# Optimization experiments

Hardware: AMD Instinct MI355X
Metric: run time of the kernel (lower is better)

Reference implementation:

```python
import jax, jax.numpy as jnp
import numpy as np

S, H = 8192, 2048


def setup_inputs() -> dict:
    key = jax.random.key(0)
    k1, k2, k3, k4, k5 = jax.random.split(key, 5)
    encoder_outputs = jax.random.normal(k1, (S, 1, H), dtype=jnp.float32)
    hidden = jax.random.normal(k2, (H,), dtype=jnp.float32)
    # nn.Linear(2H, H): weight [H, 2H], bias [H]
    lim = 1.0 / np.sqrt(2 * H)
    W_att = jax.random.uniform(k3, (H, 2 * H), dtype=jnp.float32, minval=-lim, maxval=lim)
    b_att = jax.random.uniform(k4, (H,), dtype=jnp.float32, minval=-lim, maxval=lim)
    w = jax.random.normal(k5, (1, H), dtype=jnp.float32)
    return {"encoder_outputs": encoder_outputs, "hidden": hidden,
            "W_att": W_att, "b_att": b_att, "w": w}


def reference(encoder_outputs, hidden, W_att, b_att, w):
    # Original loops over source_len: score_i = w . (Linear(cat(hidden, enc_i)))
    # Vectorized: build [S, 2H] once, one GEMM, one dot, one softmax.
    enc = encoder_outputs[:, 0, :]                      # [S, H]
    h = jnp.broadcast_to(hidden[None, :], enc.shape)    # [S, H]
    x = jnp.concatenate([h, enc], axis=1)               # [S, 2H]
    res = x @ W_att.T + b_att                           # [S, H]
    scores = res @ w[0]                                 # [S]
    attn = jax.nn.softmax(scores, axis=0)               # softmax over source_len
    return attn[None, None, :]                          # [1, 1, S]
```

## Files before the change

### kernel.cpp

```cpp
#include <hip/hip_runtime.h>
#include <math.h>

#define SS 8192
#define HH 2048
#define NBLK 256
#define NTHR 512
#define CSB 64
#define CSROWS (HH / CSB)

__device__ unsigned g_ctr = 0;
__device__ __align__(16) float g_v2[HH] = {};

__device__ __forceinline__ void grid_barrier() {
    __syncthreads();
    if (threadIdx.x == 0) {
        unsigned old = __hip_atomic_fetch_add(&g_ctr, 1u, __ATOMIC_RELAXED,
                                              __HIP_MEMORY_SCOPE_AGENT);
        unsigned target = (old / NBLK + 1u) * NBLK;
        while (__hip_atomic_load(&g_ctr, __ATOMIC_RELAXED,
                                 __HIP_MEMORY_SCOPE_AGENT) < target)
            __builtin_amdgcn_s_sleep(16);
    }
    asm volatile("" ::: "memory");
    __syncthreads();
}

__global__ __launch_bounds__(NTHR, 2) void fused_kernel(
    const float* __restrict__ enc,
    const float* __restrict__ W,
    const float* __restrict__ w,
    float* __restrict__ out,
    float* __restrict__ sc)
{
    const int b = blockIdx.x;
    const int t = threadIdx.x;

    if (b < CSB) {
        const int row0 = b * CSROWS;
        const float4* base =
            (const float4*)(W + (size_t)row0 * (2 * HH) + HH) + t;
        float4 acc = {0.f, 0.f, 0.f, 0.f};
#pragma unroll 8
        for (int j = 0; j < CSROWS; ++j) {
            float4 a = base[(size_t)j * ((2 * HH) / 4)];
            float wj = w[row0 + j];
            acc.x += wj * a.x; acc.y += wj * a.y;
            acc.z += wj * a.z; acc.w += wj * a.w;
        }
        float* dst = g_v2 + t * 4;
        atomicAdd(dst + 0, acc.x);
        atomicAdd(dst + 1, acc.y);
        atomicAdd(dst + 2, acc.z);
        atomicAdd(dst + 3, acc.w);
    }

    grid_barrier();

    __shared__ float v2s[HH];
#pragma unroll
    for (int k = 0; k < 4; ++k)
        v2s[t + k * 512] = __hip_atomic_load(&g_v2[t + k * 512],
                                             __ATOMIC_RELAXED,
                                             __HIP_MEMORY_SCOPE_AGENT);
    __syncthreads();
    {
        const int wave = t >> 6;
        const int lane = t & 63;
        const float4* v4 = (const float4*)v2s;
        float4 vf[8];
#pragma unroll
        for (int i = 0; i < 8; ++i) vf[i] = v4[lane + i * 64];

        const int row_base = b * 32 + wave * 4;
#pragma unroll
        for (int rr = 0; rr < 4; ++rr) {
            const int row = row_base + rr;
            const float4* e = (const float4*)(enc + (size_t)row * HH);
            float acc = 0.0f;
#pragma unroll
            for (int i = 0; i < 8; ++i) {
                float4 a = e[lane + i * 64];
                acc += a.x * vf[i].x + a.y * vf[i].y
                     + a.z * vf[i].z + a.w * vf[i].w;
            }
#pragma unroll
            for (int off = 32; off > 0; off >>= 1)
                acc += __shfl_down(acc, off);
            if (lane == 0)
                __hip_atomic_store(&sc[row], acc, __ATOMIC_RELAXED,
                                   __HIP_MEMORY_SCOPE_AGENT);
        }
    }

    grid_barrier();

    {
        __shared__ float red[8];
        const int lane = t & 63;
        const int wid  = t >> 6;

        float vals[16];
        float m = -INFINITY;
#pragma unroll
        for (int i = 0; i < 16; ++i) {
            vals[i] = __hip_atomic_load(&sc[t + i * 512], __ATOMIC_RELAXED,
                                        __HIP_MEMORY_SCOPE_AGENT);
            m = fmaxf(m, vals[i]);
        }
#pragma unroll
        for (int off = 1; off < 64; off <<= 1)
            m = fmaxf(m, __shfl_xor(m, off));
        if (lane == 0) red[wid] = m;
        __syncthreads();
#pragma unroll
        for (int k = 0; k < 8; ++k) m = fmaxf(m, red[k]);

        float s = 0.0f;
#pragma unroll
        for (int i = 0; i < 16; ++i)
            s += __expf(vals[i] - m);
#pragma unroll
        for (int off = 1; off < 64; off <<= 1)
            s += __shfl_xor(s, off);
        __syncthreads();
        if (lane == 0) red[wid] = s;
        __syncthreads();
        float ss = 0.0f;
#pragma unroll
        for (int k = 0; k < 8; ++k) ss += red[k];
        const float inv = 1.0f / ss;

        if (t < 32) {
            const int e = b * 32 + t;
            float sv = __hip_atomic_load(&sc[e], __ATOMIC_RELAXED,
                                         __HIP_MEMORY_SCOPE_AGENT);
            out[e] = __expf(sv - m) * inv;
        }

        if (b == NBLK - 1) {
#pragma unroll
            for (int k = 0; k < 4; ++k)
                __hip_atomic_store(&g_v2[t + k * 512], 0.0f,
                                   __ATOMIC_RELAXED,
                                   __HIP_MEMORY_SCOPE_AGENT);
        }
    }
}

extern "C" void kernel_launch(void* const* d_in, const int* in_sizes, int n_in,
                              void* d_out, int out_size, void* d_ws, size_t ws_size,
                              hipStream_t stream) {
    const float* enc   = (const float*)d_in[0];
    const float* W_att = (const float*)d_in[2];
    const float* w     = (const float*)d_in[4];

    float* out = (float*)d_out;
    float* sc  = (float*)d_ws;

    hipLaunchKernelGGL(fused_kernel, dim3(NBLK), dim3(NTHR), 0, stream,
                       enc, W_att, w, out, sc);
}
```

Baseline: 132.1 us.

## Spread W-vector reduction over all blocks and use per-block softmax partials

The W^T·w contraction is now split across all 256 blocks, each writing partial vectors to a global buffer instead of 64 blocks issuing float atomicAdds. A second grid-barrier phase then reduces those partials column-wise. The softmax now has each block compute a local max and sum, publish them as one 64-bit pair, and combine them with an online-softmax rescale, so blocks no longer re-read all 8192 scores. The grid barrier switches to a release-flag scheme that only the last arriving block writes. The cost is one extra grid barrier and a 2 MB partial buffer.

```diff
diff --git a/kernel.cpp b/kernel.cpp
--- a/kernel.cpp
+++ b/kernel.cpp
@@ -5,21 +5,27 @@
 #define HH 2048
 #define NBLK 256
 #define NTHR 512
-#define CSB 64
-#define CSROWS (HH / CSB)
 
 __device__ unsigned g_ctr = 0;
-__device__ __align__(16) float g_v2[HH] = {};
+__device__ unsigned g_rel = 0;
+__device__ float g_part[NBLK][HH];
+__device__ float g_v2[HH];
+__device__ unsigned long long g_pair[NBLK];
 
 __device__ __forceinline__ void grid_barrier() {
     __syncthreads();
     if (threadIdx.x == 0) {
         unsigned old = __hip_atomic_fetch_add(&g_ctr, 1u, __ATOMIC_RELAXED,
                                               __HIP_MEMORY_SCOPE_AGENT);
-        unsigned target = (old / NBLK + 1u) * NBLK;
-        while (__hip_atomic_load(&g_ctr, __ATOMIC_RELAXED,
-                                 __HIP_MEMORY_SCOPE_AGENT) < target)
-            __builtin_amdgcn_s_sleep(16);
+        unsigned epoch = old / NBLK;
+        if (old % NBLK == NBLK - 1u) {
+            __hip_atomic_store(&g_rel, epoch + 1u, __ATOMIC_RELAXED,
+                               __HIP_MEMORY_SCOPE_AGENT);
+        } else {
+            while (__hip_atomic_load(&g_rel, __ATOMIC_RELAXED,
+                                     __HIP_MEMORY_SCOPE_AGENT) <= epoch)
+                __builtin_amdgcn_s_sleep(8);
+        }
     }
     asm volatile("" ::: "memory");
     __syncthreads();
@@ -29,34 +35,57 @@
     const float* __restrict__ enc,
     const float* __restrict__ W,
     const float* __restrict__ w,
-    float* __restrict__ out,
-    float* __restrict__ sc)
+    float* __restrict__ out)
 {
-    const int b = blockIdx.x;
-    const int t = threadIdx.x;
+    const int b    = blockIdx.x;
+    const int t    = threadIdx.x;
+    const int wave = t >> 6;
+    const int lane = t & 63;
 
-    if (b < CSB) {
-        const int row0 = b * CSROWS;
+    __shared__ float v2s[HH];
+    __shared__ float srow[32];
+    __shared__ float mv[NBLK];
+    __shared__ float sv[NBLK];
+    __shared__ float red[2];
+
+    {
+        const int row0 = b * 8;
         const float4* base =
             (const float4*)(W + (size_t)row0 * (2 * HH) + HH) + t;
         float4 acc = {0.f, 0.f, 0.f, 0.f};
-#pragma unroll 8
-        for (int j = 0; j < CSROWS; ++j) {
+#pragma unroll
+        for (int j = 0; j < 8; ++j) {
             float4 a = base[(size_t)j * ((2 * HH) / 4)];
             float wj = w[row0 + j];
             acc.x += wj * a.x; acc.y += wj * a.y;
             acc.z += wj * a.z; acc.w += wj * a.w;
         }
-        float* dst = g_v2 + t * 4;
-        atomicAdd(dst + 0, acc.x);
-        atomicAdd(dst + 1, acc.y);
-        atomicAdd(dst + 2, acc.z);
-        atomicAdd(dst + 3, acc.w);
+        float* dst = &g_part[b][t * 4];
+        __hip_atomic_store(dst + 0, acc.x, __ATOMIC_RELAXED, __HIP_MEMORY_SCOPE_AGENT);
+        __hip_atomic_store(dst + 1, acc.y, __ATOMIC_RELAXED, __HIP_MEMORY_SCOPE_AGENT);
+        __hip_atomic_store(dst + 2, acc.z, __ATOMIC_RELAXED, __HIP_MEMORY_SCOPE_AGENT);
+        __hip_atomic_store(dst + 3, acc.w, __ATOMIC_RELAXED, __HIP_MEMORY_SCOPE_AGENT);
     }
 
     grid_barrier();
 
-    __shared__ float v2s[HH];
+    {
+        const int c = b * 8 + wave;
+        float s = 0.0f;
+#pragma unroll
+        for (int k = 0; k < 4; ++k)
+            s += __hip_atomic_load(&g_part[lane + k * 64][c],
+                                   __ATOMIC_RELAXED, __HIP_MEMORY_SCOPE_AGENT);
+#pragma unroll
+        for (int off = 32; off > 0; off >>= 1)
+            s += __shfl_down(s, off);
+        if (lane == 0)
+            __hip_atomic_store(&g_v2[c], s, __ATOMIC_RELAXED,
+                               __HIP_MEMORY_SCOPE_AGENT);
+    }
+
+    grid_barrier();
+
 #pragma unroll
     for (int k = 0; k < 4; ++k)
         v2s[t + k * 512] = __hip_atomic_load(&g_v2[t + k * 512],
@@ -64,8 +93,6 @@
                                              __HIP_MEMORY_SCOPE_AGENT);
     __syncthreads();
     {
-        const int wave = t >> 6;
-        const int lane = t & 63;
         const float4* v4 = (const float4*)v2s;
         float4 vf[8];
 #pragma unroll
@@ -86,65 +113,64 @@
 #pragma unroll
             for (int off = 32; off > 0; off >>= 1)
                 acc += __shfl_down(acc, off);
-            if (lane == 0)
-                __hip_atomic_store(&sc[row], acc, __ATOMIC_RELAXED,
-                                   __HIP_MEMORY_SCOPE_AGENT);
+            if (lane == 0) srow[wave * 4 + rr] = acc;
+        }
+    }
+    __syncthreads();
+
+    if (wave == 0) {
+        float v = (lane < 32) ? srow[lane] : -INFINITY;
+        float m = v;
+#pragma unroll
+        for (int off = 1; off < 64; off <<= 1)
+            m = fmaxf(m, __shfl_xor(m, off));
+        float s = (lane < 32) ? __expf(v - m) : 0.0f;
+#pragma unroll
+        for (int off = 1; off < 64; off <<= 1)
+            s += __shfl_xor(s, off);
+        if (lane == 0) {
+            unsigned long long p =
+                ((unsigned long long)__float_as_uint(s) << 32) |
+                (unsigned long long)__float_as_uint(m);
+            __hip_atomic_store(&g_pair[b], p, __ATOMIC_RELAXED,
+                               __HIP_MEMORY_SCOPE_AGENT);
         }
     }
 
     grid_barrier();
 
-    {
-        __shared__ float red[8];
-        const int lane = t & 63;
-        const int wid  = t >> 6;
+    if (t < NBLK) {
+        unsigned long long p = __hip_atomic_load(&g_pair[t], __ATOMIC_RELAXED,
+                                                 __HIP_MEMORY_SCOPE_AGENT);
+        mv[t] = __uint_as_float((unsigned)(p & 0xffffffffu));
+        sv[t] = __uint_as_float((unsigned)(p >> 32));
+    }
+    __syncthreads();
+    if (wave == 0) {
+        float m4 = fmaxf(fmaxf(mv[lane], mv[lane + 64]),
+                         fmaxf(mv[lane + 128], mv[lane + 192]));
+#pragma unroll
+        for (int off = 32; off > 0; off >>= 1)
+            m4 = fmaxf(m4, __shfl_xor(m4, off));
+        if (lane == 0) red[0] = m4;
+    }
+    __syncthreads();
+    const float M = red[0];
+    if (wave == 0) {
+        float s4 = sv[lane]       * __expf(mv[lane]       - M)
+                 + sv[lane + 64]  * __expf(mv[lane + 64]  - M)
+                 + sv[lane + 128] * __expf(mv[lane + 128] - M)
+                 + sv[lane + 192] * __expf(mv[lane + 192] - M);
+#pragma unroll
+        for (int off = 32; off > 0; off >>= 1)
+            s4 += __shfl_xor(s4, off);
+        if (lane == 0) red[1] = s4;
+    }
+    __syncthreads();
+    const float inv = 1.0f / red[1];
 
-        float vals[16];
-        float m = -INFINITY;
-#pragma unroll
-        for (int i = 0; i < 16; ++i) {
-            vals[i] = __hip_atomic_load(&sc[t + i * 512], __ATOMIC_RELAXED,
-                                        __HIP_MEMORY_SCOPE_AGENT);
-            m = fmaxf(m, vals[i]);
-        }
-#pragma unroll
-        for (int off = 1; off < 64; off <<= 1)
-            m = fmaxf(m, __shfl_xor(m, off));
-        if (lane == 0) red[wid] = m;
-        __syncthreads();
-#pragma unroll
-        for (int k = 0; k < 8; ++k) m = fmaxf(m, red[k]);
-
-        float s = 0.0f;
-#pragma unroll
-        for (int i = 0; i < 16; ++i)
-            s += __expf(vals[i] - m);
-#pragma unroll
-        for (int off = 1; off < 64; off <<= 1)
-            s += __shfl_xor(s, off);
-        __syncthreads();
-        if (lane == 0) red[wid] = s;
-        __syncthreads();
-        float ss = 0.0f;
-#pragma unroll
-        for (int k = 0; k < 8; ++k) ss += red[k];
-        const float inv = 1.0f / ss;
-
-        if (t < 32) {
-            const int e = b * 32 + t;
-            float sv = __hip_atomic_load(&sc[e], __ATOMIC_RELAXED,
-                                         __HIP_MEMORY_SCOPE_AGENT);
-            out[e] = __expf(sv - m) * inv;
-        }
-
-        if (b == NBLK - 1) {
-#pragma unroll
-            for (int k = 0; k < 4; ++k)
-                __hip_atomic_store(&g_v2[t + k * 512], 0.0f,
-                                   __ATOMIC_RELAXED,
-                                   __HIP_MEMORY_SCOPE_AGENT);
-        }
-    }
+    if (t < 32)
+        out[b * 32 + t] = __expf(srow[t] - M) * inv;
 }
 
 extern "C" void kernel_launch(void* const* d_in, const int* in_sizes, int n_in,
@@ -155,8 +181,7 @@
     const float* w     = (const float*)d_in[4];
 
     float* out = (float*)d_out;
-    float* sc  = (float*)d_ws;
 
     hipLaunchKernelGGL(fused_kernel, dim3(NBLK), dim3(NTHR), 0, stream,
-                       enc, W_att, w, out, sc);
+                       enc, W_att, w, out);
 }
```

Result: slower. 142.4 us (+7.8%).
